# Kernel tuning notes

Measured on AMD Instinct MI355X. Metric: run time of the kernel, lower is better.

## Reference

```python
import jax, jax.numpy as jnp
import numpy as np

IMG = 256
CUT_RATE = 0.1
CUT_LEN = int(IMG * CUT_RATE)      # 25
REMAIN = (IMG - CUT_LEN) // 2      # 115
CROP = 2 * REMAIN                  # 230  (crop window is always CROP x CROP)


def _cut_start(index):
    # vectorized cut_location(); window length is always CROP, return left edge a
    xy = IMG - index
    return jnp.where(index <= REMAIN, 0,
           jnp.where(xy <= REMAIN, IMG - CROP, index - REMAIN)).astype(jnp.int32)


def _bilinear_crop(img, x0, y0):
    # img: [C, IMG, IMG]; crop CROP x CROP window at (x0, y0) and resize to
    # IMG x IMG with bilinear, align_corners=True (matches F.interpolate).
    scale = (CROP - 1) / (IMG - 1)
    src = jnp.arange(IMG, dtype=img.dtype) * scale        # [IMG] source coords in crop
    i0 = jnp.floor(src).astype(jnp.int32)
    i1 = jnp.minimum(i0 + 1, CROP - 1)
    w = src - i0.astype(img.dtype)                        # [IMG] frac weights
    r0, r1 = x0 + i0, x0 + i1                             # absolute row indices
    c0, c1 = y0 + i0, y0 + i1                             # absolute col indices
    top = img[:, r0, :]                                   # [C, IMG, IMG]
    bot = img[:, r1, :]
    rows = top * (1.0 - w)[None, :, None] + bot * w[None, :, None]
    left = rows[:, :, c0]
    right = rows[:, :, c1]
    return left * (1.0 - w)[None, None, :] + right * w[None, None, :]


def setup_inputs() -> dict:
    key = jax.random.key(0)
    k1, k2 = jax.random.split(key)
    x = jax.random.normal(k1, (128, 3, 256, 256), dtype=jnp.float32)
    feature_map = jax.random.normal(k2, (128, 512, 16, 16), dtype=jnp.float32)
    return {"x": x, "feature_map": feature_map}


def reference(x, feature_map):
    B, C, H, W = feature_map.shape
    # SE-style weighting: global avg pool per channel, relu(weight * fm)
    fw = feature_map.mean(axis=(2, 3), keepdims=True)     # [B,C,1,1]
    se = jax.nn.relu(fw * feature_map)                    # [B,C,H,W]
    cam = se.mean(axis=1)                                 # [B,H,W] channel-mean CAM
    idx = jnp.argmax(cam.reshape(B, -1), axis=1)          # flat argmax per sample
    fx = idx // H                                         # torch uses feature_size[0]
    fy = idx % W
    ix = (IMG * fx) // H                                  # map to image coords
    iy = (IMG * fy) // W
    x_left = _cut_start(ix)
    y_top = _cut_start(iy)
    out = jax.vmap(_bilinear_crop)(x, x_left, y_top)      # [B,3,256,256]
    # torch clones+detaches the crop; output carries no gradient
    return jax.lax.stop_gradient(out)
```

## Files before the change

### kernel.cpp

```cpp
#include <hip/hip_runtime.h>

#define IMG 256
#define CROPW 230
#define REMAIN 115
#define NGROUP 16
#define GCH    32
#define TILE_I 16
#define MAXROWS 16
#define NTILE  16

__device__ __forceinline__ int cut_start(int v) {
    int xy = IMG - v;
    return (v <= REMAIN) ? 0 : ((xy <= REMAIN) ? (IMG - CROPW) : (v - REMAIN));
}

__global__ __launch_bounds__(256) void cam_partial_kernel(
    const float* __restrict__ fm, float* __restrict__ cam_part)
{
    const int blk = blockIdx.x;
    const int b = blk >> 4;
    const int g = blk & (NGROUP - 1);
    const int tid = threadIdx.x;
    const int lane = tid & 63;
    const int wave = tid >> 6;

    __shared__ float tile[GCH * 256];
    __shared__ float fw[GCH];

    const float* src = fm + ((size_t)b * 512 + (size_t)g * GCH) * 256;

    const float4* src4 = (const float4*)src;
    float4* tile4 = (float4*)tile;
    #pragma unroll
    for (int k = 0; k < 8; ++k)
        tile4[tid + k * 256] = src4[tid + k * 256];
    __syncthreads();

    for (int c = wave * 8; c < wave * 8 + 8; ++c) {
        const float* row = tile + c * 256;
        float s = row[lane] + row[lane + 64] + row[lane + 128] + row[lane + 192];
        #pragma unroll
        for (int off = 32; off >= 1; off >>= 1)
            s += __shfl_xor(s, off, 64);
        if (lane == 0) fw[c] = s * (1.0f / 256.0f);
    }
    __syncthreads();

    float acc = 0.0f;
    #pragma unroll
    for (int c = 0; c < GCH; ++c) {
        float v = fw[c] * tile[c * 256 + tid];
        acc += (v > 0.0f) ? v : 0.0f;
    }
    cam_part[(size_t)blk * 256 + tid] = acc;
}

__global__ __launch_bounds__(256) void argmax_kernel(
    const float* __restrict__ cam_part, int* __restrict__ se_out)
{
    const int b = blockIdx.x;
    const int tid = threadIdx.x;

    __shared__ float s_val[256];
    __shared__ int   s_idx[256];

    float acc = 0.0f;
    #pragma unroll
    for (int g = 0; g < NGROUP; ++g)
        acc += cam_part[((size_t)b * NGROUP + g) * 256 + tid];

    s_val[tid] = acc;
    s_idx[tid] = tid;
    __syncthreads();

    for (int stride = 128; stride >= 1; stride >>= 1) {
        if (tid < stride) {
            float v2 = s_val[tid + stride]; int i2 = s_idx[tid + stride];
            float v1 = s_val[tid];          int i1 = s_idx[tid];
            if (v2 > v1 || (v2 == v1 && i2 < i1)) { s_val[tid] = v2; s_idx[tid] = i2; }
        }
        __syncthreads();
    }

    if (tid == 0) {
        int idx = s_idx[0];
        int fx = idx >> 4, fy = idx & 15;
        int ix = 16 * fx,  iy = 16 * fy;
        se_out[2 * b]     = cut_start(ix);
        se_out[2 * b + 1] = cut_start(iy);
    }
}

__global__ __launch_bounds__(256) void bilinear_tiled_kernel(
    const float* __restrict__ x, const int* __restrict__ se, float* __restrict__ out)
{
    __shared__ float rows[MAXROWS * 256];

    const int bx = blockIdx.x;
    const int bc = bx >> 4;
    const int ib = (bx & 15) * TILE_I;
    const int b  = bc / 3;
    const int tid = threadIdx.x;

    const int x0 = se[2 * b];
    const int y0 = se[2 * b + 1];

    const float scale = (float)(229.0 / 255.0);

    const int i0_first = (int)floorf((float)ib * scale);
    const int i0_last  = (int)floorf((float)(ib + TILE_I - 1) * scale);
    const int r_first  = x0 + i0_first;
    const int r_last   = x0 + min(i0_last + 1, CROPW - 1);
    const int nrows    = r_last - r_first + 1;

    const float4* src4 = (const float4*)(x + (size_t)bc * (IMG * IMG) + (size_t)r_first * IMG);
    float4* rows4 = (float4*)rows;
    for (int k = tid; k < nrows * (IMG / 4); k += 256)
        rows4[k] = src4[k];
    __syncthreads();

    const int j = tid;
    const float sj = (float)j * scale;
    const int   j0 = (int)floorf(sj);
    const float wj = sj - (float)j0;
    const int   j1 = min(j0 + 1, CROPW - 1);
    const int   c0 = y0 + j0;
    const int   c1 = y0 + j1;
    const float owj = 1.0f - wj;

    float* outp = out + (size_t)bc * (IMG * IMG) + (size_t)ib * IMG + j;

    #pragma unroll
    for (int il = 0; il < TILE_I; ++il) {
        const int i = ib + il;
        const float si = (float)i * scale;
        const int   i0 = (int)floorf(si);
        const float wi = si - (float)i0;
        const int   i1 = min(i0 + 1, CROPW - 1);
        const int   row0 = (x0 + i0 - r_first) << 8;
        const int   row1 = (x0 + i1 - r_first) << 8;

        const float A  = rows[row0 + c0];
        const float Bv = rows[row0 + c1];
        const float C  = rows[row1 + c0];
        const float D  = rows[row1 + c1];

        const float l = A  * (1.0f - wi) + C * wi;
        const float r = Bv * (1.0f - wi) + D * wi;
        outp[il * IMG] = l * owj + r * wj;
    }
}

extern "C" void kernel_launch(void* const* d_in, const int* in_sizes, int n_in,
                              void* d_out, int out_size, void* d_ws, size_t ws_size,
                              hipStream_t stream) {
    const float* x  = (const float*)d_in[0];
    const float* fm = (const float*)d_in[1];
    float* out = (float*)d_out;

    int*   se       = (int*)d_ws;
    float* cam_part = (float*)((char*)d_ws + 1024);

    cam_partial_kernel<<<128 * NGROUP, 256, 0, stream>>>(fm, cam_part);
    argmax_kernel<<<128, 256, 0, stream>>>(cam_part, se);

    bilinear_tiled_kernel<<<384 * NTILE, 256, 0, stream>>>(x, se, out);
}
```

Measured before the change: 55.56 us.

## Process three tiles per block with register-prefetched next tile rows

The bilinear kernel now has each block handle three consecutive tiles. It loads the next tile's rows from global memory into registers while it computes the current tile out of shared memory, then stores the prefetched rows to shared memory after a barrier. Each tile always loads a fixed 16 rows, clamped at the image edge, which gives a static vectorized load pattern. The aim is to hide global load latency and cut the number of blocks launched, at the cost of extra registers, extra barriers and fewer blocks (2048) to fill the GPU.

```diff
diff --git a/kernel.cpp b/kernel.cpp
--- a/kernel.cpp
+++ b/kernel.cpp
@@ -8,6 +8,7 @@
 #define TILE_I 16
 #define MAXROWS 16
 #define NTILE  16
+#define TPB    3
 
 __device__ __forceinline__ int cut_start(int v) {
     int xy = IMG - v;
@@ -91,63 +92,92 @@
     }
 }
 
-__global__ __launch_bounds__(256) void bilinear_tiled_kernel(
+__global__ __launch_bounds__(256) void bilinear_pipe_kernel(
     const float* __restrict__ x, const int* __restrict__ se, float* __restrict__ out)
 {
     __shared__ float rows[MAXROWS * 256];
+    float4* rows4 = (float4*)rows;
 
-    const int bx = blockIdx.x;
-    const int bc = bx >> 4;
-    const int ib = (bx & 15) * TILE_I;
-    const int b  = bc / 3;
-    const int tid = threadIdx.x;
-
-    const int x0 = se[2 * b];
-    const int y0 = se[2 * b + 1];
-
+    const int tid  = threadIdx.x;
+    const int wave = tid >> 6;
+    const int lane = tid & 63;
     const float scale = (float)(229.0 / 255.0);
 
-    const int i0_first = (int)floorf((float)ib * scale);
-    const int i0_last  = (int)floorf((float)(ib + TILE_I - 1) * scale);
-    const int r_first  = x0 + i0_first;
-    const int r_last   = x0 + min(i0_last + 1, CROPW - 1);
-    const int nrows    = r_last - r_first + 1;
+    const int t0 = blockIdx.x * TPB;
 
-    const float4* src4 = (const float4*)(x + (size_t)bc * (IMG * IMG) + (size_t)r_first * IMG);
-    float4* rows4 = (float4*)rows;
-    for (int k = tid; k < nrows * (IMG / 4); k += 256)
-        rows4[k] = src4[k];
+    auto tile_params = [&](int t, int& bc, int& ib, int& x0, int& y0, int& r_first) {
+        bc = t >> 4;
+        ib = (t & (NTILE - 1)) * TILE_I;
+        const int b = bc / 3;
+        x0 = se[2 * b];
+        y0 = se[2 * b + 1];
+        const int i0f = (int)floorf((float)ib * scale);
+        r_first = x0 + i0f;
+    };
+
+    auto load_tile = [&](int t, float4 st[4]) {
+        int bc, ib, x0, y0, r_first;
+        tile_params(t, bc, ib, x0, y0, r_first);
+        const float4* img4 = (const float4*)(x + (size_t)bc * (IMG * IMG));
+        #pragma unroll
+        for (int k = 0; k < 4; ++k) {
+            const int row  = 4 * k + wave;
+            const int srow = min(r_first + row, IMG - 1);
+            st[k] = img4[srow * 64 + lane];
+        }
+    };
+
+    float4 st[4];
+    load_tile(t0, st);
+    #pragma unroll
+    for (int k = 0; k < 4; ++k) rows4[tid + k * 256] = st[k];
     __syncthreads();
 
-    const int j = tid;
-    const float sj = (float)j * scale;
-    const int   j0 = (int)floorf(sj);
-    const float wj = sj - (float)j0;
-    const int   j1 = min(j0 + 1, CROPW - 1);
-    const int   c0 = y0 + j0;
-    const int   c1 = y0 + j1;
-    const float owj = 1.0f - wj;
+    for (int it = 0; it < TPB; ++it) {
+        const int t = t0 + it;
+        int bc, ib, x0, y0, r_first;
+        tile_params(t, bc, ib, x0, y0, r_first);
 
-    float* outp = out + (size_t)bc * (IMG * IMG) + (size_t)ib * IMG + j;
+        float4 nx[4];
+        if (it + 1 < TPB) load_tile(t + 1, nx);
 
-    #pragma unroll
-    for (int il = 0; il < TILE_I; ++il) {
-        const int i = ib + il;
-        const float si = (float)i * scale;
-        const int   i0 = (int)floorf(si);
-        const float wi = si - (float)i0;
-        const int   i1 = min(i0 + 1, CROPW - 1);
-        const int   row0 = (x0 + i0 - r_first) << 8;
-        const int   row1 = (x0 + i1 - r_first) << 8;
+        const int   j  = tid;
+        const float sj = (float)j * scale;
+        const int   j0 = (int)floorf(sj);
+        const float wj = sj - (float)j0;
+        const int   j1 = min(j0 + 1, CROPW - 1);
+        const int   c0 = y0 + j0;
+        const int   c1 = y0 + j1;
+        const float owj = 1.0f - wj;
 
-        const float A  = rows[row0 + c0];
-        const float Bv = rows[row0 + c1];
-        const float C  = rows[row1 + c0];
-        const float D  = rows[row1 + c1];
+        float* outp = out + (size_t)bc * (IMG * IMG) + (size_t)ib * IMG + j;
 
-        const float l = A  * (1.0f - wi) + C * wi;
-        const float r = Bv * (1.0f - wi) + D * wi;
-        outp[il * IMG] = l * owj + r * wj;
+        #pragma unroll
+        for (int il = 0; il < TILE_I; ++il) {
+            const int   i  = ib + il;
+            const float si = (float)i * scale;
+            const int   i0 = (int)floorf(si);
+            const float wi = si - (float)i0;
+            const int   i1 = min(i0 + 1, CROPW - 1);
+            const int   row0 = (x0 + i0 - r_first) << 8;
+            const int   row1 = (x0 + i1 - r_first) << 8;
+
+            const float A  = rows[row0 + c0];
+            const float Bv = rows[row0 + c1];
+            const float C  = rows[row1 + c0];
+            const float D  = rows[row1 + c1];
+
+            const float l = A  * (1.0f - wi) + C * wi;
+            const float r = Bv * (1.0f - wi) + D * wi;
+            outp[il * IMG] = l * owj + r * wj;
+        }
+        __syncthreads();
+
+        if (it + 1 < TPB) {
+            #pragma unroll
+            for (int k = 0; k < 4; ++k) rows4[tid + k * 256] = nx[k];
+            __syncthreads();
+        }
     }
 }
 
@@ -164,5 +194,5 @@
     cam_partial_kernel<<<128 * NGROUP, 256, 0, stream>>>(fm, cam_part);
     argmax_kernel<<<128, 256, 0, stream>>>(cam_part, se);
 
-    bilinear_tiled_kernel<<<384 * NTILE, 256, 0, stream>>>(x, se, out);
+    bilinear_pipe_kernel<<<2048, 256, 0, stream>>>(x, se, out);
 }
```

New measurement: 83.14 us. 1.5x slower.
